# Performance work log

Measured on AMD Instinct MI355X. Metric: run time of the kernel, lower is better.

## Reference

```python
import jax, jax.numpy as jnp
import numpy as np

WIDTH = 256
HEAD = 16
SCALE = 2
G = WIDTH // HEAD          # 16 groups
NH = G * SCALE             # 32 kernelized heads
EPS = 1e-5
N_NODES = 20000
B_GRAPHS = 1024


def setup_inputs() -> dict:
    key = jax.random.key(0)
    ks = jax.random.split(key, 10)
    x = jax.random.normal(ks[0], (N_NODES, WIDTH), jnp.float32)
    x_res = jax.random.normal(ks[1], (B_GRAPHS, NH, HEAD, HEAD), jnp.float32)
    batch = jnp.sort(jax.random.randint(ks[2], (N_NODES,), 0, B_GRAPHS)).astype(jnp.int64)
    w_pre = jax.random.normal(ks[3], (WIDTH, WIDTH), jnp.float32) * 0.02
    b_pre = jnp.zeros((WIDTH,), jnp.float32)
    # grouped 1x1 convs: [groups, width_scale, head_out, head_in]
    wq = jax.random.normal(ks[4], (G, SCALE, HEAD, HEAD), jnp.float32) * 0.02
    wk = jax.random.normal(ks[5], (G, SCALE, HEAD, HEAD), jnp.float32) * 0.02
    wv = jax.random.normal(ks[6], (G, SCALE, HEAD, HEAD), jnp.float32) * 0.02
    w_post = jax.random.normal(ks[7], (WIDTH, WIDTH * SCALE), jnp.float32) * 0.02
    b_post = jnp.zeros((WIDTH,), jnp.float32)
    log_scale = jnp.full((WIDTH,), np.log(0.01), jnp.float32)
    return {"x": x, "x_res": x_res, "batch": batch, "batch_size": B_GRAPHS,
            "w_pre": w_pre, "b_pre": b_pre, "wq": wq, "wk": wk, "wv": wv,
            "w_post": w_post, "b_post": b_post, "log_scale": log_scale}


def reference(x, x_res, batch, batch_size, w_pre, b_pre, wq, wk, wv, w_post, b_post, log_scale):
    n = x.shape[0]
    # pre: 1x1 conv (= linear) + GroupNorm(affine=False); L=1 so normalize over
    # each group's width_head channels.
    y = x @ w_pre.T + b_pre                       # [N, width]
    yg = y.reshape(n, G, HEAD)                    # [N, G, Hd]
    mu = yg.mean(-1, keepdims=True)
    var = yg.var(-1, keepdims=True)               # biased, as in GroupNorm
    yn = (yg - mu) / jnp.sqrt(var + EPS)          # [N, G, Hd]

    inv_sqrt_h = 1.0 / np.sqrt(HEAD)
    # grouped convs -> kernelized q,k (exp) and v
    xq = jnp.exp(jnp.einsum('ngi,gsoi->ngso', yn, wq) * inv_sqrt_h).reshape(n, NH, HEAD)
    xk = jnp.exp(jnp.einsum('ngi,gsoi->ngso', yn, wk) * inv_sqrt_h).reshape(n, NH, HEAD)
    xv = jnp.einsum('ngi,gsoi->ngso', yn, wv).reshape(n, NH, HEAD)

    # outer product k (x) v then scatter-sum over graphs  [B, NH, Hd, Hd]
    kv = jnp.einsum('bnh,bnv->bnhv', xk, xv)
    kv_sum = jax.ops.segment_sum(kv, batch, num_segments=batch_size) + x_res
    x_res_out = kv_sum

    # per-graph key sum, gathered back to nodes
    k_sum = jax.ops.segment_sum(xk, batch, num_segments=batch_size)[batch]  # [N, NH, Hd]
    denom = jnp.einsum('bnh,bnh->bn', xq, k_sum)                            # [N, NH]
    qn = xq / denom[:, :, None]

    out = jnp.einsum('bnh,bnhv->bnv', qn, kv_sum[batch]).reshape(n, WIDTH * SCALE)
    out = jnp.exp(log_scale) * (out @ w_post.T + b_post)                    # [N, width]
    return (out, x_res_out)
```

## Files before the change

kernel.cpp:

```cpp
#include <hip/hip_runtime.h>
#include <stdint.h>

typedef unsigned int u32;
typedef unsigned short u16;
typedef __attribute__((ext_vector_type(8))) short v8s;
typedef __attribute__((ext_vector_type(4))) float v4f;

#define GN_EPS 1e-5f

__device__ __forceinline__ float bflo(u32 u){ return __uint_as_float(u << 16); }
__device__ __forceinline__ float bfhi(u32 u){ return __uint_as_float(u & 0xffff0000u); }
__device__ __forceinline__ u16 f2bf(float f){
  u32 x = __float_as_uint(f);
  u32 r = (x + 0x7fffu + ((x >> 16) & 1u)) >> 16;
  return (u16)r;
}
__device__ __forceinline__ u32 pack2(float a, float b){
  return (u32)f2bf(a) | ((u32)f2bf(b) << 16);
}
__device__ __forceinline__ void unpack8(const uint4 u, float* f){
  f[0]=bflo(u.x); f[1]=bfhi(u.x); f[2]=bflo(u.y); f[3]=bfhi(u.y);
  f[4]=bflo(u.z); f[5]=bfhi(u.z); f[6]=bflo(u.w); f[7]=bfhi(u.w);
}
__device__ __forceinline__ uint4 loadpack8(const float* __restrict__ p){
  float4 a = *(const float4*)p, b = *(const float4*)(p + 4);
  return make_uint4(pack2(a.x,a.y),pack2(a.z,a.w),pack2(b.x,b.y),pack2(b.z,b.w));
}

__device__ __forceinline__ int getb(const int* __restrict__ b, int is64, int i){
  return b[is64 ? 2*i : i];
}

__global__ __launch_bounds__(256) void k_detect(
    const int* __restrict__ batch, int n, int* __restrict__ flags)
{
  int i = blockIdx.x*256 + threadIdx.x;
  int bad = 0;
  if (i < n - 1 && batch[i] > batch[i + 1]) bad = 1;
  if (__builtin_amdgcn_ballot_w64(bad) != 0 && (threadIdx.x & 63) == 0)
    atomicOr(&flags[0], 1);
}

__global__ __launch_bounds__(256) void k_bounds(
    const int* __restrict__ batch, const int* __restrict__ flags,
    int N, int B, int* __restrict__ bounds)
{
  int i = blockIdx.x*256 + threadIdx.x;
  if (i >= N) return;
  const int is64 = flags[0];
  int b = getb(batch, is64, i);
  int prev = (i == 0) ? -1 : getb(batch, is64, i - 1);
  for (int g = prev + 1; g <= b; g++) bounds[g] = i;
  if (i == N - 1)
    for (int g = b + 1; g <= B; g++) bounds[g] = N;
}

__global__ __launch_bounds__(256) void k_pre(
    const float* __restrict__ x, const float* __restrict__ wpre,
    const float* __restrict__ bpre, float* __restrict__ y, int N, int nbm)
{
  __shared__ __align__(16) u16 As[64*40];
  __shared__ __align__(16) u16 Bs[64*40];
  const int t = threadIdx.x;
  const int bm = blockIdx.x % nbm;
  const int bn = blockIdx.x / nbm;
  const int m_base = bm*64, n_base = bn*64;
  const int w = t >> 6, lane = t & 63;
  const int wm = (w >> 1)*32, wn = (w & 1)*32;
  const int fr = lane & 15, fk = lane >> 4;
  const int srow = t >> 2, scol = (t & 3)*8;

  v4f acc[2][2];
#pragma unroll
  for (int i = 0; i < 2; i++)
#pragma unroll
    for (int j = 0; j < 2; j++) acc[i][j] = (v4f){0.f,0.f,0.f,0.f};

  for (int k0 = 0; k0 < 256; k0 += 32) {
    __syncthreads();
    {
      int gm = m_base + srow;
      uint4 av = make_uint4(0u,0u,0u,0u);
      if (gm < N) av = loadpack8(x + (size_t)gm*256 + k0 + scol);
      *(uint4*)&As[srow*40 + scol] = av;
      uint4 bv = loadpack8(wpre + (size_t)(n_base + srow)*256 + k0 + scol);
      *(uint4*)&Bs[srow*40 + scol] = bv;
    }
    __syncthreads();
    v8s a0 = *(const v8s*)&As[(wm      + fr)*40 + fk*8];
    v8s a1 = *(const v8s*)&As[(wm + 16 + fr)*40 + fk*8];
    v8s b0 = *(const v8s*)&Bs[(wn      + fr)*40 + fk*8];
    v8s b1 = *(const v8s*)&Bs[(wn + 16 + fr)*40 + fk*8];
    acc[0][0] = __builtin_amdgcn_mfma_f32_16x16x32_bf16(a0,b0,acc[0][0],0,0,0);
    acc[0][1] = __builtin_amdgcn_mfma_f32_16x16x32_bf16(a0,b1,acc[0][1],0,0,0);
    acc[1][0] = __builtin_amdgcn_mfma_f32_16x16x32_bf16(a1,b0,acc[1][0],0,0,0);
    acc[1][1] = __builtin_amdgcn_mfma_f32_16x16x32_bf16(a1,b1,acc[1][1],0,0,0);
  }
#pragma unroll
  for (int nj = 0; nj < 2; nj++) {
    int col = n_base + wn + nj*16 + fr;
    float bpv = bpre[col];
#pragma unroll
    for (int mi = 0; mi < 2; mi++) {
#pragma unroll
      for (int r = 0; r < 4; r++) {
        int row = m_base + wm + mi*16 + fk*4 + r;
        if (row < N) y[(size_t)row*256 + col] = acc[mi][nj][r] + bpv;
      }
    }
  }
}

__global__ __launch_bounds__(256) void k_gnqkv(
    const float* __restrict__ y, const float* __restrict__ wq,
    const float* __restrict__ wk, const float* __restrict__ wv,
    u16* __restrict__ qo, u16* __restrict__ ko, u16* __restrict__ vo, int N)
{
  __shared__ __align__(16) float wL[3*512];
  const int t = threadIdx.x;
  const int g = blockIdx.x & 15;
  const int c = blockIdx.x >> 4;
  {
    const float* srcs[3] = {wq, wk, wv};
#pragma unroll
    for (int tz = 0; tz < 3; tz++) {
      wL[tz*512 + t]       = srcs[tz][g*512 + t];
      wL[tz*512 + t + 256] = srcs[tz][g*512 + t + 256];
    }
  }
  __syncthreads();
  const int node = c*256 + t;
  if (node >= N) return;

  const float* yp = y + (size_t)node*256 + g*16;
  float4 v0 = *(const float4*)yp;
  float4 v1 = *(const float4*)(yp + 4);
  float4 v2 = *(const float4*)(yp + 8);
  float4 v3 = *(const float4*)(yp + 12);
  float a[16] = {v0.x,v0.y,v0.z,v0.w, v1.x,v1.y,v1.z,v1.w,
                 v2.x,v2.y,v2.z,v2.w, v3.x,v3.y,v3.z,v3.w};
  float mu = 0.f;
#pragma unroll
  for (int i = 0; i < 16; i++) mu += a[i];
  mu *= 0.0625f;
  float s2 = 0.f;
#pragma unroll
  for (int i = 0; i < 16; i++) { float d = a[i]-mu; s2 = fmaf(d,d,s2); }
  float inv = rsqrtf(s2*0.0625f + GN_EPS);
  float yn[16];
#pragma unroll
  for (int i = 0; i < 16; i++) yn[i] = (a[i]-mu)*inv;

  u16* outs[3] = {qo, ko, vo};
#pragma unroll
  for (int tz = 0; tz < 3; tz++) {
#pragma unroll
    for (int s = 0; s < 2; s++) {
      u32 p[8];
#pragma unroll
      for (int o = 0; o < 16; o++) {
        const float* row = &wL[tz*512 + (s*16 + o)*16];
        float4 W0 = *(const float4*)row;
        float4 W1 = *(const float4*)(row + 4);
        float4 W2 = *(const float4*)(row + 8);
        float4 W3 = *(const float4*)(row + 12);
        float w[16] = {W0.x,W0.y,W0.z,W0.w,W1.x,W1.y,W1.z,W1.w,
                       W2.x,W2.y,W2.z,W2.w,W3.x,W3.y,W3.z,W3.w};
        float d = 0.f;
#pragma unroll
        for (int i = 0; i < 16; i++) d = fmaf(yn[i], w[i], d);
        if (tz < 2) d = __expf(d*0.25f);
        if (o & 1) p[o>>1] |= (u32)f2bf(d) << 16;
        else       p[o>>1]  = (u32)f2bf(d);
      }
      u16* dst = outs[tz] + (size_t)node*512 + g*32 + s*16;
      *(uint4*)dst       = make_uint4(p[0],p[1],p[2],p[3]);
      *(uint4*)(dst + 8) = make_uint4(p[4],p[5],p[6],p[7]);
    }
  }
}

__global__ __launch_bounds__(256) void k_segatt(
    const u16* __restrict__ xk, const u16* __restrict__ xv,
    const u16* __restrict__ xq, const float* __restrict__ xres,
    const int* __restrict__ bounds,
    float* __restrict__ out1, u16* __restrict__ att, int N)
{
  __shared__ __align__(16) u16 kvs[32*280];
  __shared__ float kss[32*17];
  const int b = blockIdx.x, t = threadIdx.x;
  const int lo = bounds[b], hi = bounds[b+1];
  const int nh = t >> 3, hp = t & 7;

  float kv[2][16];
#pragma unroll
  for (int r = 0; r < 2; r++)
#pragma unroll
    for (int v = 0; v < 16; v++) kv[r][v] = 0.f;
  float ks0 = 0.f, ks1 = 0.f;

  const size_t koff = (size_t)nh*16 + 2*hp;
  const size_t voff = (size_t)nh*16;
  for (int node = lo; node < hi; node++) {
    u32 kw = *(const u32*)(xk + (size_t)node*512 + koff);
    uint4 V0 = *(const uint4*)(xv + (size_t)node*512 + voff);
    uint4 V1 = *(const uint4*)(xv + (size_t)node*512 + voff + 8);
    float k0 = bflo(kw), k1 = bfhi(kw);
    float vf[16]; unpack8(V0, vf); unpack8(V1, vf + 8);
    ks0 += k0; ks1 += k1;
#pragma unroll
    for (int v = 0; v < 16; v++) {
      kv[0][v] = fmaf(k0, vf[v], kv[0][v]);
      kv[1][v] = fmaf(k1, vf[v], kv[1][v]);
    }
  }
  kss[nh*17 + 2*hp]     = ks0;
  kss[nh*17 + 2*hp + 1] = ks1;

#pragma unroll
  for (int r = 0; r < 2; r++) {
    int h = 2*hp + r;
    size_t idx = ((size_t)(b*32 + nh)*16 + h)*16;
    const float* xp = xres + idx;
    float4 X0 = *(const float4*)xp;
    float4 X1 = *(const float4*)(xp + 4);
    float4 X2 = *(const float4*)(xp + 8);
    float4 X3 = *(const float4*)(xp + 12);
    float xf[16] = {X0.x,X0.y,X0.z,X0.w,X1.x,X1.y,X1.z,X1.w,
                    X2.x,X2.y,X2.z,X2.w,X3.x,X3.y,X3.z,X3.w};
    float o[16];
#pragma unroll
    for (int j = 0; j < 16; j++) o[j] = kv[r][j] + xf[j];
    float* op = out1 + idx;
    *(float4*)op        = make_float4(o[0],o[1],o[2],o[3]);
    *(float4*)(op + 4)  = make_float4(o[4],o[5],o[6],o[7]);
    *(float4*)(op + 8)  = make_float4(o[8],o[9],o[10],o[11]);
    *(float4*)(op + 12) = make_float4(o[12],o[13],o[14],o[15]);
    u16* lp = &kvs[nh*280 + h*16];
    *(uint4*)lp       = make_uint4(pack2(o[0],o[1]),  pack2(o[2],o[3]),
                                   pack2(o[4],o[5]),  pack2(o[6],o[7]));
    *(uint4*)(lp + 8) = make_uint4(pack2(o[8],o[9]),  pack2(o[10],o[11]),
                                   pack2(o[12],o[13]),pack2(o[14],o[15]));
  }
  __syncthreads();

  const int nh2 = t & 31, ns = t >> 5;
  for (int n0 = lo; n0 < hi; n0 += 8) {
    int node = n0 + ns;
    if (node >= hi) continue;
    const u16* qp = xq + (size_t)node*512 + nh2*16;
    uint4 Q0 = *(const uint4*)qp;
    uint4 Q1 = *(const uint4*)(qp + 8);
    float q[16]; unpack8(Q0, q); unpack8(Q1, q + 8);
    const float* ksp = &kss[nh2*17];
    float denom = 0.f;
#pragma unroll
    for (int i = 0; i < 16; i++) denom = fmaf(q[i], ksp[i], denom);
    float inv = 1.0f / fmaxf(denom, 1e-20f);
    float a[16];
#pragma unroll
    for (int v = 0; v < 16; v++) a[v] = 0.f;
    const u16* kvp = &kvs[nh2*280];
#pragma unroll
    for (int h = 0; h < 16; h++) {
      float qh = q[h] * inv;
      uint4 W0 = *(const uint4*)(kvp + h*16);
      uint4 W1 = *(const uint4*)(kvp + h*16 + 8);
      float w[16]; unpack8(W0, w); unpack8(W1, w + 8);
#pragma unroll
      for (int v = 0; v < 16; v++) a[v] = fmaf(qh, w[v], a[v]);
    }
    u32 p[8];
#pragma unroll
    for (int j = 0; j < 8; j++) p[j] = pack2(a[2*j], a[2*j+1]);
    u16* dst = att + (size_t)node*512 + nh2*16;
    *(uint4*)dst       = make_uint4(p[0],p[1],p[2],p[3]);
    *(uint4*)(dst + 8) = make_uint4(p[4],p[5],p[6],p[7]);
  }
}

__global__ __launch_bounds__(256) void k_post(
    const u16* __restrict__ att, const float* __restrict__ wpost,
    const float* __restrict__ bpost, const float* __restrict__ ls,
    float* __restrict__ out0, int N, int nbm)
{
  __shared__ __align__(16) u16 As[64*40];
  __shared__ __align__(16) u16 Bs[64*40];
  const int t = threadIdx.x;
  const int bm = blockIdx.x % nbm;
  const int bn = blockIdx.x / nbm;
  const int m_base = bm*64, n_base = bn*64;
  const int w = t >> 6, lane = t & 63;
  const int wm = (w >> 1)*32, wn = (w & 1)*32;
  const int fr = lane & 15, fk = lane >> 4;
  const int srow = t >> 2, scol = (t & 3)*8;

  v4f acc[2][2];
#pragma unroll
  for (int i = 0; i < 2; i++)
#pragma unroll
    for (int j = 0; j < 2; j++) acc[i][j] = (v4f){0.f,0.f,0.f,0.f};

  for (int k0 = 0; k0 < 512; k0 += 32) {
    __syncthreads();
    {
      int gm = m_base + srow;
      uint4 av = make_uint4(0u,0u,0u,0u);
      if (gm < N) av = *(const uint4*)(att + (size_t)gm*512 + k0 + scol);
      *(uint4*)&As[srow*40 + scol] = av;
      uint4 bv = loadpack8(wpost + (size_t)(n_base + srow)*512 + k0 + scol);
      *(uint4*)&Bs[srow*40 + scol] = bv;
    }
    __syncthreads();
    v8s a0 = *(const v8s*)&As[(wm      + fr)*40 + fk*8];
    v8s a1 = *(const v8s*)&As[(wm + 16 + fr)*40 + fk*8];
    v8s b0 = *(const v8s*)&Bs[(wn      + fr)*40 + fk*8];
    v8s b1 = *(const v8s*)&Bs[(wn + 16 + fr)*40 + fk*8];
    acc[0][0] = __builtin_amdgcn_mfma_f32_16x16x32_bf16(a0,b0,acc[0][0],0,0,0);
    acc[0][1] = __builtin_amdgcn_mfma_f32_16x16x32_bf16(a0,b1,acc[0][1],0,0,0);
    acc[1][0] = __builtin_amdgcn_mfma_f32_16x16x32_bf16(a1,b0,acc[1][0],0,0,0);
    acc[1][1] = __builtin_amdgcn_mfma_f32_16x16x32_bf16(a1,b1,acc[1][1],0,0,0);
  }
#pragma unroll
  for (int nj = 0; nj < 2; nj++) {
    int col = n_base + wn + nj*16 + fr;
    float bpv = bpost[col];
    float e   = __expf(ls[col]);
#pragma unroll
    for (int mi = 0; mi < 2; mi++) {
#pragma unroll
      for (int r = 0; r < 4; r++) {
        int row = m_base + wm + mi*16 + fk*4 + r;
        if (row < N) out0[(size_t)row*256 + col] = e*(acc[mi][nj][r] + bpv);
      }
    }
  }
}

extern "C" void kernel_launch(void* const* d_in, const int* in_sizes, int n_in,
                              void* d_out, int out_size, void* d_ws, size_t ws_size,
                              hipStream_t stream)
{
  const float* x     = (const float*)d_in[0];
  const float* xres  = (const float*)d_in[1];
  const int*   batch = (const int*)d_in[2];
  const float* wpre  = (const float*)d_in[4];
  const float* bpre  = (const float*)d_in[5];
  const float* wq    = (const float*)d_in[6];
  const float* wk    = (const float*)d_in[7];
  const float* wv    = (const float*)d_in[8];
  const float* wpost = (const float*)d_in[9];
  const float* bpost = (const float*)d_in[10];
  const float* ls    = (const float*)d_in[11];

  const int N = in_sizes[0] / 256;
  const int B = in_sizes[1] / 8192;
  const int nbm = (N + 63) / 64;
  const int nchunk = (N + 255) / 256;

  char* ws = (char*)d_ws;
  size_t off = 0;
  int*   flags  = (int*)(ws + off); off += 256;
  int*   bounds = (int*)(ws + off); off += ((size_t)B + 64) * 4;
  float* y      = (float*)(ws + off);
  u16*   att    = (u16*)(ws + off);  off += (size_t)N * 1024;
  u16*   q      = (u16*)(ws + off);  off += (size_t)N * 1024;
  u16*   kten   = (u16*)(ws + off);  off += (size_t)N * 1024;
  u16*   vten   = (u16*)(ws + off);  off += (size_t)N * 1024;

  float* out0 = (float*)d_out;
  float* out1 = out0 + (size_t)N * 256;

  hipMemsetAsync(flags, 0, 4, stream);
  k_detect<<<nchunk,         256, 0, stream>>>(batch, N, flags);
  k_bounds<<<nchunk,         256, 0, stream>>>(batch, flags, N, B, bounds);
  k_pre   <<<nbm * 4,        256, 0, stream>>>(x, wpre, bpre, y, N, nbm);
  k_gnqkv <<<nchunk * 16,    256, 0, stream>>>(y, wq, wk, wv, q, kten, vten, N);
  k_segatt<<<B,              256, 0, stream>>>(kten, vten, q, xres, bounds,
                                               out1, att, N);
  k_post  <<<nbm * 4,        256, 0, stream>>>(att, wpost, bpost, ls, out0, N, nbm);
}
```

Before: 135.9 us.

## Split per-graph KV accumulation across two thread halves with LDS reduction

The segment-attention kernel now runs 512 threads per graph. Two halves each accumulate the k⊗v outer products over alternating nodes, with two nodes unrolled per iteration so more loads are in flight, and the partial sums are then reduced through shared memory. The second phase now processes 16 nodes per iteration instead of 8. The aim is to shorten the serial per-node loop, which with roughly 20 nodes per graph limits latency. In exchange it adds about 42KB of LDS, an extra barrier, and larger blocks, which may reduce occupancy.

```diff
diff --git a/kernel.cpp b/kernel.cpp
--- a/kernel.cpp
+++ b/kernel.cpp
@@ -180,17 +180,20 @@
   }
 }
 
-__global__ __launch_bounds__(256) void k_segatt(
+__global__ __launch_bounds__(512) void k_segatt(
     const u16* __restrict__ xk, const u16* __restrict__ xv,
     const u16* __restrict__ xq, const float* __restrict__ xres,
     const int* __restrict__ bounds,
     float* __restrict__ out1, u16* __restrict__ att, int N)
 {
+  __shared__ __align__(16) float red[512*20];
+  __shared__ __align__(16) float kspart[512];
   __shared__ __align__(16) u16 kvs[32*280];
   __shared__ float kss[32*17];
   const int b = blockIdx.x, t = threadIdx.x;
   const int lo = bounds[b], hi = bounds[b+1];
-  const int nh = t >> 3, hp = t & 7;
+  const int half = t >> 8;
+  const int nh = (t >> 3) & 31, hp = t & 7;
 
   float kv[2][16];
 #pragma unroll
@@ -201,8 +204,30 @@
 
   const size_t koff = (size_t)nh*16 + 2*hp;
   const size_t voff = (size_t)nh*16;
-  for (int node = lo; node < hi; node++) {
-    u32 kw = *(const u32*)(xk + (size_t)node*512 + koff);
+  int node = lo + half;
+  for (; node + 2 < hi; node += 4) {
+    u32  kw0 = *(const u32*) (xk + (size_t)node*512 + koff);
+    uint4 Va0 = *(const uint4*)(xv + (size_t)node*512 + voff);
+    uint4 Va1 = *(const uint4*)(xv + (size_t)node*512 + voff + 8);
+    u32  kw1 = *(const u32*) (xk + (size_t)(node+2)*512 + koff);
+    uint4 Vb0 = *(const uint4*)(xv + (size_t)(node+2)*512 + voff);
+    uint4 Vb1 = *(const uint4*)(xv + (size_t)(node+2)*512 + voff + 8);
+    float a0 = bflo(kw0), a1 = bfhi(kw0);
+    float b0 = bflo(kw1), b1 = bfhi(kw1);
+    float va[16], vb[16];
+    unpack8(Va0, va); unpack8(Va1, va + 8);
+    unpack8(Vb0, vb); unpack8(Vb1, vb + 8);
+    ks0 += a0 + b0; ks1 += a1 + b1;
+#pragma unroll
+    for (int v = 0; v < 16; v++) {
+      kv[0][v] = fmaf(a0, va[v], kv[0][v]);
+      kv[1][v] = fmaf(a1, va[v], kv[1][v]);
+      kv[0][v] = fmaf(b0, vb[v], kv[0][v]);
+      kv[1][v] = fmaf(b1, vb[v], kv[1][v]);
+    }
+  }
+  if (node < hi) {
+    u32  kw = *(const u32*) (xk + (size_t)node*512 + koff);
     uint4 V0 = *(const uint4*)(xv + (size_t)node*512 + voff);
     uint4 V1 = *(const uint4*)(xv + (size_t)node*512 + voff + 8);
     float k0 = bflo(kw), k1 = bfhi(kw);
@@ -214,41 +239,72 @@
       kv[1][v] = fmaf(k1, vf[v], kv[1][v]);
     }
   }
-  kss[nh*17 + 2*hp]     = ks0;
-  kss[nh*17 + 2*hp + 1] = ks1;
-
-#pragma unroll
-  for (int r = 0; r < 2; r++) {
-    int h = 2*hp + r;
-    size_t idx = ((size_t)(b*32 + nh)*16 + h)*16;
-    const float* xp = xres + idx;
-    float4 X0 = *(const float4*)xp;
-    float4 X1 = *(const float4*)(xp + 4);
-    float4 X2 = *(const float4*)(xp + 8);
-    float4 X3 = *(const float4*)(xp + 12);
-    float xf[16] = {X0.x,X0.y,X0.z,X0.w,X1.x,X1.y,X1.z,X1.w,
-                    X2.x,X2.y,X2.z,X2.w,X3.x,X3.y,X3.z,X3.w};
-    float o[16];
-#pragma unroll
-    for (int j = 0; j < 16; j++) o[j] = kv[r][j] + xf[j];
-    float* op = out1 + idx;
-    *(float4*)op        = make_float4(o[0],o[1],o[2],o[3]);
-    *(float4*)(op + 4)  = make_float4(o[4],o[5],o[6],o[7]);
-    *(float4*)(op + 8)  = make_float4(o[8],o[9],o[10],o[11]);
-    *(float4*)(op + 12) = make_float4(o[12],o[13],o[14],o[15]);
-    u16* lp = &kvs[nh*280 + h*16];
-    *(uint4*)lp       = make_uint4(pack2(o[0],o[1]),  pack2(o[2],o[3]),
-                                   pack2(o[4],o[5]),  pack2(o[6],o[7]));
-    *(uint4*)(lp + 8) = make_uint4(pack2(o[8],o[9]),  pack2(o[10],o[11]),
-                                   pack2(o[12],o[13]),pack2(o[14],o[15]));
+
+  if (half == 0) {
+#pragma unroll
+    for (int r = 0; r < 2; r++) {
+      float* rp = &red[(nh*16 + 2*hp + r)*20];
+      *(float4*)rp       = make_float4(kv[r][0], kv[r][1], kv[r][2], kv[r][3]);
+      *(float4*)(rp + 4) = make_float4(kv[r][4], kv[r][5], kv[r][6], kv[r][7]);
+      *(float4*)(rp + 8) = make_float4(kv[r][8], kv[r][9], kv[r][10],kv[r][11]);
+      *(float4*)(rp + 12)= make_float4(kv[r][12],kv[r][13],kv[r][14],kv[r][15]);
+    }
+    kspart[nh*16 + 2*hp]     = ks0;
+    kspart[nh*16 + 2*hp + 1] = ks1;
   }
   __syncthreads();
 
+  if (half == 1) {
+#pragma unroll
+    for (int r = 0; r < 2; r++) {
+      const float* rp = &red[(nh*16 + 2*hp + r)*20];
+      float4 R0 = *(const float4*)rp;
+      float4 R1 = *(const float4*)(rp + 4);
+      float4 R2 = *(const float4*)(rp + 8);
+      float4 R3 = *(const float4*)(rp + 12);
+      kv[r][0] += R0.x; kv[r][1] += R0.y; kv[r][2] += R0.z; kv[r][3] += R0.w;
+      kv[r][4] += R1.x; kv[r][5] += R1.y; kv[r][6] += R1.z; kv[r][7] += R1.w;
+      kv[r][8] += R2.x; kv[r][9] += R2.y; kv[r][10]+= R2.z; kv[r][11]+= R2.w;
+      kv[r][12]+= R3.x; kv[r][13]+= R3.y; kv[r][14]+= R3.z; kv[r][15]+= R3.w;
+    }
+    ks0 += kspart[nh*16 + 2*hp];
+    ks1 += kspart[nh*16 + 2*hp + 1];
+    kss[nh*17 + 2*hp]     = ks0;
+    kss[nh*17 + 2*hp + 1] = ks1;
+
+#pragma unroll
+    for (int r = 0; r < 2; r++) {
+      int h = 2*hp + r;
+      size_t idx = ((size_t)(b*32 + nh)*16 + h)*16;
+      const float* xp = xres + idx;
+      float4 X0 = *(const float4*)xp;
+      float4 X1 = *(const float4*)(xp + 4);
+      float4 X2 = *(const float4*)(xp + 8);
+      float4 X3 = *(const float4*)(xp + 12);
+      float xf[16] = {X0.x,X0.y,X0.z,X0.w,X1.x,X1.y,X1.z,X1.w,
+                      X2.x,X2.y,X2.z,X2.w,X3.x,X3.y,X3.z,X3.w};
+      float o[16];
+#pragma unroll
+      for (int j = 0; j < 16; j++) o[j] = kv[r][j] + xf[j];
+      float* op = out1 + idx;
+      *(float4*)op        = make_float4(o[0],o[1],o[2],o[3]);
+      *(float4*)(op + 4)  = make_float4(o[4],o[5],o[6],o[7]);
+      *(float4*)(op + 8)  = make_float4(o[8],o[9],o[10],o[11]);
+      *(float4*)(op + 12) = make_float4(o[12],o[13],o[14],o[15]);
+      u16* lp = &kvs[nh*280 + h*16];
+      *(uint4*)lp       = make_uint4(pack2(o[0],o[1]),  pack2(o[2],o[3]),
+                                     pack2(o[4],o[5]),  pack2(o[6],o[7]));
+      *(uint4*)(lp + 8) = make_uint4(pack2(o[8],o[9]),  pack2(o[10],o[11]),
+                                     pack2(o[12],o[13]),pack2(o[14],o[15]));
+    }
+  }
+  __syncthreads();
+
   const int nh2 = t & 31, ns = t >> 5;
-  for (int n0 = lo; n0 < hi; n0 += 8) {
-    int node = n0 + ns;
-    if (node >= hi) continue;
-    const u16* qp = xq + (size_t)node*512 + nh2*16;
+  for (int n0 = lo; n0 < hi; n0 += 16) {
+    int nodei = n0 + ns;
+    if (nodei >= hi) continue;
+    const u16* qp = xq + (size_t)nodei*512 + nh2*16;
     uint4 Q0 = *(const uint4*)qp;
     uint4 Q1 = *(const uint4*)(qp + 8);
     float q[16]; unpack8(Q0, q); unpack8(Q1, q + 8);
@@ -273,7 +329,7 @@
     u32 p[8];
 #pragma unroll
     for (int j = 0; j < 8; j++) p[j] = pack2(a[2*j], a[2*j+1]);
-    u16* dst = att + (size_t)node*512 + nh2*16;
+    u16* dst = att + (size_t)nodei*512 + nh2*16;
     *(uint4*)dst       = make_uint4(p[0],p[1],p[2],p[3]);
     *(uint4*)(dst + 8) = make_uint4(p[4],p[5],p[6],p[7]);
   }
@@ -376,7 +432,7 @@
   k_bounds<<<nchunk,         256, 0, stream>>>(batch, flags, N, B, bounds);
   k_pre   <<<nbm * 4,        256, 0, stream>>>(x, wpre, bpre, y, N, nbm);
   k_gnqkv <<<nchunk * 16,    256, 0, stream>>>(y, wq, wk, wv, q, kten, vten, N);
-  k_segatt<<<B,              256, 0, stream>>>(kten, vten, q, xres, bounds,
+  k_segatt<<<B,              512, 0, stream>>>(kten, vten, q, xres, bounds,
                                                out1, att, N);
   k_post  <<<nbm * 4,        256, 0, stream>>>(att, wpost, bpost, ls, out0, N, nbm);
 }
```

Measured after the change: 135.2 us. No clear change (-0.6%).

## Split segment attention across head quarters and node-parallel slices with LDS reduction

Applied to the files above, without the earlier changes.

The segment-attention kernel now launches four blocks per graph, each handling 8 of the 32 heads. Within a block, four node slices accumulate k⊗v partials in parallel, with a one-step register prefetch of the next node's loads. The partials are then combined through a two-stage shared-memory tree reduction. This targets the serial per-graph node loop (about 20 nodes per graph) and raises the block count. In exchange it adds extra syncs and shared-memory traffic, and each head quarter reads its K/V/Q slices separately.

```diff
diff --git a/kernel.cpp b/kernel.cpp
--- a/kernel.cpp
+++ b/kernel.cpp
@@ -186,11 +186,15 @@
     const int* __restrict__ bounds,
     float* __restrict__ out1, u16* __restrict__ att, int N)
 {
-  __shared__ __align__(16) u16 kvs[32*280];
-  __shared__ float kss[32*17];
-  const int b = blockIdx.x, t = threadIdx.x;
+  __shared__ __align__(16) float red[2*2592];
+  __shared__ float ksred[2*130];
+  __shared__ __align__(16) u16 kvsL[8*280];
+  __shared__ float kssL[8*17];
+  const int t = threadIdx.x;
+  const int b  = blockIdx.x >> 2;
+  const int H0 = (blockIdx.x & 3) * 8;
   const int lo = bounds[b], hi = bounds[b+1];
-  const int nh = t >> 3, hp = t & 7;
+  const int ns = t >> 6, nh = (t >> 3) & 7, hp = t & 7;
 
   float kv[2][16];
 #pragma unroll
@@ -199,12 +203,23 @@
     for (int v = 0; v < 16; v++) kv[r][v] = 0.f;
   float ks0 = 0.f, ks1 = 0.f;
 
-  const size_t koff = (size_t)nh*16 + 2*hp;
-  const size_t voff = (size_t)nh*16;
-  for (int node = lo; node < hi; node++) {
-    u32 kw = *(const u32*)(xk + (size_t)node*512 + koff);
-    uint4 V0 = *(const uint4*)(xv + (size_t)node*512 + voff);
-    uint4 V1 = *(const uint4*)(xv + (size_t)node*512 + voff + 8);
+  const size_t koff = (size_t)(H0 + nh)*16 + 2*hp;
+  const size_t voff = (size_t)(H0 + nh)*16;
+  int node = lo + ns;
+  u32 kw = 0; uint4 V0 = make_uint4(0,0,0,0), V1 = make_uint4(0,0,0,0);
+  if (node < hi) {
+    kw = *(const u32*) (xk + (size_t)node*512 + koff);
+    V0 = *(const uint4*)(xv + (size_t)node*512 + voff);
+    V1 = *(const uint4*)(xv + (size_t)node*512 + voff + 8);
+  }
+  while (node < hi) {
+    int nxt = node + 4;
+    u32 kwn = 0; uint4 V0n = make_uint4(0,0,0,0), V1n = make_uint4(0,0,0,0);
+    if (nxt < hi) {
+      kwn = *(const u32*) (xk + (size_t)nxt*512 + koff);
+      V0n = *(const uint4*)(xv + (size_t)nxt*512 + voff);
+      V1n = *(const uint4*)(xv + (size_t)nxt*512 + voff + 8);
+    }
     float k0 = bflo(kw), k1 = bfhi(kw);
     float vf[16]; unpack8(V0, vf); unpack8(V1, vf + 8);
     ks0 += k0; ks1 += k1;
@@ -213,46 +228,109 @@
       kv[0][v] = fmaf(k0, vf[v], kv[0][v]);
       kv[1][v] = fmaf(k1, vf[v], kv[1][v]);
     }
-  }
-  kss[nh*17 + 2*hp]     = ks0;
-  kss[nh*17 + 2*hp + 1] = ks1;
-
-#pragma unroll
-  for (int r = 0; r < 2; r++) {
-    int h = 2*hp + r;
-    size_t idx = ((size_t)(b*32 + nh)*16 + h)*16;
-    const float* xp = xres + idx;
-    float4 X0 = *(const float4*)xp;
-    float4 X1 = *(const float4*)(xp + 4);
-    float4 X2 = *(const float4*)(xp + 8);
-    float4 X3 = *(const float4*)(xp + 12);
-    float xf[16] = {X0.x,X0.y,X0.z,X0.w,X1.x,X1.y,X1.z,X1.w,
-                    X2.x,X2.y,X2.z,X2.w,X3.x,X3.y,X3.z,X3.w};
-    float o[16];
-#pragma unroll
-    for (int j = 0; j < 16; j++) o[j] = kv[r][j] + xf[j];
-    float* op = out1 + idx;
-    *(float4*)op        = make_float4(o[0],o[1],o[2],o[3]);
-    *(float4*)(op + 4)  = make_float4(o[4],o[5],o[6],o[7]);
-    *(float4*)(op + 8)  = make_float4(o[8],o[9],o[10],o[11]);
-    *(float4*)(op + 12) = make_float4(o[12],o[13],o[14],o[15]);
-    u16* lp = &kvs[nh*280 + h*16];
-    *(uint4*)lp       = make_uint4(pack2(o[0],o[1]),  pack2(o[2],o[3]),
-                                   pack2(o[4],o[5]),  pack2(o[6],o[7]));
-    *(uint4*)(lp + 8) = make_uint4(pack2(o[8],o[9]),  pack2(o[10],o[11]),
-                                   pack2(o[12],o[13]),pack2(o[14],o[15]));
+    kw = kwn; V0 = V0n; V1 = V1n; node = nxt;
+  }
+
+  if (ns >= 2) {
+    float* s = &red[(ns - 2)*2592];
+#pragma unroll
+    for (int r = 0; r < 2; r++) {
+      float* rp = &s[nh*324 + (2*hp + r)*20];
+      *(float4*)rp       = make_float4(kv[r][0], kv[r][1], kv[r][2], kv[r][3]);
+      *(float4*)(rp + 4) = make_float4(kv[r][4], kv[r][5], kv[r][6], kv[r][7]);
+      *(float4*)(rp + 8) = make_float4(kv[r][8], kv[r][9], kv[r][10],kv[r][11]);
+      *(float4*)(rp + 12)= make_float4(kv[r][12],kv[r][13],kv[r][14],kv[r][15]);
+    }
+    ksred[(ns-2)*130 + nh*16 + 2*hp]     = ks0;
+    ksred[(ns-2)*130 + nh*16 + 2*hp + 1] = ks1;
   }
   __syncthreads();
-
-  const int nh2 = t & 31, ns = t >> 5;
-  for (int n0 = lo; n0 < hi; n0 += 8) {
-    int node = n0 + ns;
-    if (node >= hi) continue;
-    const u16* qp = xq + (size_t)node*512 + nh2*16;
+  if (ns < 2) {
+    const float* s = &red[ns*2592];
+#pragma unroll
+    for (int r = 0; r < 2; r++) {
+      const float* rp = &s[nh*324 + (2*hp + r)*20];
+      float4 R0 = *(const float4*)rp;
+      float4 R1 = *(const float4*)(rp + 4);
+      float4 R2 = *(const float4*)(rp + 8);
+      float4 R3 = *(const float4*)(rp + 12);
+      kv[r][0] += R0.x; kv[r][1] += R0.y; kv[r][2] += R0.z; kv[r][3] += R0.w;
+      kv[r][4] += R1.x; kv[r][5] += R1.y; kv[r][6] += R1.z; kv[r][7] += R1.w;
+      kv[r][8] += R2.x; kv[r][9] += R2.y; kv[r][10]+= R2.z; kv[r][11]+= R2.w;
+      kv[r][12]+= R3.x; kv[r][13]+= R3.y; kv[r][14]+= R3.z; kv[r][15]+= R3.w;
+    }
+    ks0 += ksred[ns*130 + nh*16 + 2*hp];
+    ks1 += ksred[ns*130 + nh*16 + 2*hp + 1];
+  }
+  __syncthreads();
+  if (ns == 1) {
+#pragma unroll
+    for (int r = 0; r < 2; r++) {
+      float* rp = &red[nh*324 + (2*hp + r)*20];
+      *(float4*)rp       = make_float4(kv[r][0], kv[r][1], kv[r][2], kv[r][3]);
+      *(float4*)(rp + 4) = make_float4(kv[r][4], kv[r][5], kv[r][6], kv[r][7]);
+      *(float4*)(rp + 8) = make_float4(kv[r][8], kv[r][9], kv[r][10],kv[r][11]);
+      *(float4*)(rp + 12)= make_float4(kv[r][12],kv[r][13],kv[r][14],kv[r][15]);
+    }
+    ksred[nh*16 + 2*hp]     = ks0;
+    ksred[nh*16 + 2*hp + 1] = ks1;
+  }
+  __syncthreads();
+  if (ns == 0) {
+#pragma unroll
+    for (int r = 0; r < 2; r++) {
+      const float* rp = &red[nh*324 + (2*hp + r)*20];
+      float4 R0 = *(const float4*)rp;
+      float4 R1 = *(const float4*)(rp + 4);
+      float4 R2 = *(const float4*)(rp + 8);
+      float4 R3 = *(const float4*)(rp + 12);
+      kv[r][0] += R0.x; kv[r][1] += R0.y; kv[r][2] += R0.z; kv[r][3] += R0.w;
+      kv[r][4] += R1.x; kv[r][5] += R1.y; kv[r][6] += R1.z; kv[r][7] += R1.w;
+      kv[r][8] += R2.x; kv[r][9] += R2.y; kv[r][10]+= R2.z; kv[r][11]+= R2.w;
+      kv[r][12]+= R3.x; kv[r][13]+= R3.y; kv[r][14]+= R3.z; kv[r][15]+= R3.w;
+    }
+    ks0 += ksred[nh*16 + 2*hp];
+    ks1 += ksred[nh*16 + 2*hp + 1];
+    kssL[nh*17 + 2*hp]     = ks0;
+    kssL[nh*17 + 2*hp + 1] = ks1;
+
+#pragma unroll
+    for (int r = 0; r < 2; r++) {
+      int h = 2*hp + r;
+      size_t idx = ((size_t)(b*32 + H0 + nh)*16 + h)*16;
+      const float* xp = xres + idx;
+      float4 X0 = *(const float4*)xp;
+      float4 X1 = *(const float4*)(xp + 4);
+      float4 X2 = *(const float4*)(xp + 8);
+      float4 X3 = *(const float4*)(xp + 12);
+      float xf[16] = {X0.x,X0.y,X0.z,X0.w,X1.x,X1.y,X1.z,X1.w,
+                      X2.x,X2.y,X2.z,X2.w,X3.x,X3.y,X3.z,X3.w};
+      float o[16];
+#pragma unroll
+      for (int j = 0; j < 16; j++) o[j] = kv[r][j] + xf[j];
+      float* op = out1 + idx;
+      *(float4*)op        = make_float4(o[0],o[1],o[2],o[3]);
+      *(float4*)(op + 4)  = make_float4(o[4],o[5],o[6],o[7]);
+      *(float4*)(op + 8)  = make_float4(o[8],o[9],o[10],o[11]);
+      *(float4*)(op + 12) = make_float4(o[12],o[13],o[14],o[15]);
+      u16* lp = &kvsL[nh*280 + h*16];
+      *(uint4*)lp       = make_uint4(pack2(o[0],o[1]),  pack2(o[2],o[3]),
+                                     pack2(o[4],o[5]),  pack2(o[6],o[7]));
+      *(uint4*)(lp + 8) = make_uint4(pack2(o[8],o[9]),  pack2(o[10],o[11]),
+                                     pack2(o[12],o[13]),pack2(o[14],o[15]));
+    }
+  }
+  __syncthreads();
+
+  const int nh2 = t & 7, ns2 = t >> 3;
+  for (int n0 = lo; n0 < hi; n0 += 32) {
+    int nodei = n0 + ns2;
+    if (nodei >= hi) continue;
+    const u16* qp = xq + (size_t)nodei*512 + (H0 + nh2)*16;
     uint4 Q0 = *(const uint4*)qp;
     uint4 Q1 = *(const uint4*)(qp + 8);
     float q[16]; unpack8(Q0, q); unpack8(Q1, q + 8);
-    const float* ksp = &kss[nh2*17];
+    const float* ksp = &kssL[nh2*17];
     float denom = 0.f;
 #pragma unroll
     for (int i = 0; i < 16; i++) denom = fmaf(q[i], ksp[i], denom);
@@ -260,7 +338,7 @@
     float a[16];
 #pragma unroll
     for (int v = 0; v < 16; v++) a[v] = 0.f;
-    const u16* kvp = &kvs[nh2*280];
+    const u16* kvp = &kvsL[nh2*280];
 #pragma unroll
     for (int h = 0; h < 16; h++) {
       float qh = q[h] * inv;
@@ -273,7 +351,7 @@
     u32 p[8];
 #pragma unroll
     for (int j = 0; j < 8; j++) p[j] = pack2(a[2*j], a[2*j+1]);
-    u16* dst = att + (size_t)node*512 + nh2*16;
+    u16* dst = att + (size_t)nodei*512 + (H0 + nh2)*16;
     *(uint4*)dst       = make_uint4(p[0],p[1],p[2],p[3]);
     *(uint4*)(dst + 8) = make_uint4(p[4],p[5],p[6],p[7]);
   }
@@ -376,7 +454,7 @@
   k_bounds<<<nchunk,         256, 0, stream>>>(batch, flags, N, B, bounds);
   k_pre   <<<nbm * 4,        256, 0, stream>>>(x, wpre, bpre, y, N, nbm);
   k_gnqkv <<<nchunk * 16,    256, 0, stream>>>(y, wq, wk, wv, q, kten, vten, N);
-  k_segatt<<<B,              256, 0, stream>>>(kten, vten, q, xres, bounds,
+  k_segatt<<<B * 4,          256, 0, stream>>>(kten, vten, q, xres, bounds,
                                                out1, att, N);
   k_post  <<<nbm * 4,        256, 0, stream>>>(att, wpost, bpost, ls, out0, N, nbm);
 }
```

Measured after the change: 136.4 us. No clear change (+0.3%).
